# Optimization experiments

Hardware: AMD Instinct MI355X
Metric: run time of the kernel (lower is better)

Reference implementation:

```python
import jax, jax.numpy as jnp
import numpy as np

B = 512
N = 8732  # SSD300 default box count, hard-coded in the original asserts


def point_form(boxes):
    # (cx, cy, w, h) -> (xmin, ymin, xmax, ymax), as in the original repo
    return jnp.concatenate([boxes[..., :2] - boxes[..., 2:] / 2,
                            boxes[..., :2] + boxes[..., 2:] / 2], axis=-1)


def setup_inputs() -> dict:
    key = jax.random.key(0)
    k1, k2, k3, k4, k5 = jax.random.split(key, 5)
    ploc = jax.random.normal(k1, (B, 4, N), jnp.float32)
    pconf = jax.random.normal(k2, (B, 2, N), jnp.float32)
    # ground-truth boxes: keep w/h strictly positive for the log in _to_offsets
    gloc = jax.random.uniform(k3, (B, N, 4), jnp.float32, minval=0.05, maxval=1.0)
    glabel = (jax.random.uniform(k4, (B, N)) < 0.02).astype(jnp.int32)
    # default boxes in cxcywh; keep away from 0 so point_form xmax/ymax > 0
    dboxes = jax.random.uniform(k5, (N, 4), jnp.float32, minval=0.2, maxval=0.8)
    return {"ploc": ploc, "pconf": pconf, "gloc": gloc, "glabel": glabel, "dboxes": dboxes}


def reference(ploc, pconf, gloc, glabel, dboxes):
    db = point_form(dboxes)                      # [N,4]
    dxy, dwh = db[:, :2], db[:, 2:]              # faithful to original indexing
    # offset encode ground truth
    gxy = (gloc[..., :2] - dxy) / dwh            # [B,N,2]
    gwh = jnp.log(gloc[..., 2:] / dwh)           # [B,N,2]
    goff = jnp.concatenate([gxy, gwh], axis=-1)  # [B,N,4]

    pl = jnp.swapaxes(ploc, 1, 2)                # [B,N,4]
    diff = pl - goff
    ad = jnp.abs(diff)
    sl1 = jnp.where(ad < 1.0, 0.5 * diff * diff, ad - 0.5).sum(-1)  # [B,N]

    mask = glabel > 0                            # [B,N]
    pos = mask.sum(axis=1)                       # [B]
    loc_loss = jnp.where(mask, sl1, 0.0).sum(axis=1)

    # per-anchor cross entropy over the class dim
    logp = jax.nn.log_softmax(pconf, axis=1)     # [B,2,N]
    closs = -jnp.take_along_axis(logp, glabel[:, None, :], axis=1)[:, 0, :]  # [B,N]

    # hard negative mining: rank negatives by loss via double argsort
    con_neg = jnp.where(mask, 0.0, closs)
    con_idx = jnp.argsort(-con_neg, axis=1)
    con_rank = jnp.argsort(con_idx, axis=1)
    neg_num = jnp.minimum(3 * pos, N)[:, None]
    neg_mask = con_rank < neg_num
    w = mask.astype(closs.dtype) + neg_mask.astype(closs.dtype)
    con_loss = (closs * w).sum(axis=1)

    total = loc_loss + con_loss
    num_mask = (pos > 0).astype(total.dtype)
    posf = jnp.maximum(pos.astype(total.dtype), 1e-6)
    return (total * num_mask / posf).mean()
```

## Files before the change

### kernel.cpp

```cpp
#include <hip/hip_runtime.h>
#include <cstdint>

#define BLOCK 1024
#define NWAVES (BLOCK/64)
#define NHIST 8
#define B_SZ 512
#define N_SZ 8732
#define NG (N_SZ/4)

__device__ __forceinline__ float f4c(const float4& v, int j) {
  return j==0 ? v.x : (j==1 ? v.y : (j==2 ? v.z : v.w));
}
__device__ __forceinline__ int i4c(const int4& v, int j) {
  return j==0 ? v.x : (j==1 ? v.y : (j==2 ? v.z : v.w));
}
__device__ __forceinline__ float smoothl1(float d) {
  float ad = fabsf(d);
  return ad < 1.0f ? 0.5f*d*d : ad - 0.5f;
}

__global__ __launch_bounds__(BLOCK, 8)
void mbl_row_kernel(const float* __restrict__ ploc,
                    const float* __restrict__ pconf,
                    const float* __restrict__ gloc,
                    const int*   __restrict__ glabel,
                    const float* __restrict__ dboxes,
                    float* __restrict__ rowout)
{
  __shared__ __align__(16) uint32_t con[N_SZ];
  __shared__ uint32_t hist[NHIST*256];
  __shared__ float redf[NWAVES], redf2[NWAVES];
  __shared__ int   redi[NWAVES];
  __shared__ int sh_pos, sh_rem;
  __shared__ uint32_t sh_prefix;
  __shared__ float sh_loc, sh_pcl;

  const int b    = blockIdx.x;
  const int tid  = threadIdx.x;
  const int wid  = tid >> 6;
  const int lane = tid & 63;

  const float* pl  = ploc  + (size_t)b * (4*N_SZ);
  const float* pc  = pconf + (size_t)b * (2*N_SZ);
  const float4* gl4  = (const float4*)(gloc   + (size_t)b * (N_SZ*4));
  const int4*   lab4 = (const int4*)  (glabel + (size_t)b * N_SZ);
  const float4* db4  = (const float4*)dboxes;

  for (int i = tid; i < NHIST*256; i += BLOCK) hist[i] = 0u;
  __syncthreads();

  float loc_acc = 0.f, pcl_acc = 0.f;
  int pos_acc = 0;
  uint32_t* hmy = hist + (wid & (NHIST-1))*256;

  for (int g = tid; g < NG; g += BLOCK) {
    const int n = g*4;
    float4 pl0 = *(const float4*)(pl + n);
    float4 pl1 = *(const float4*)(pl + N_SZ   + n);
    float4 pl2 = *(const float4*)(pl + 2*N_SZ + n);
    float4 pl3 = *(const float4*)(pl + 3*N_SZ + n);
    float4 pc0 = *(const float4*)(pc + n);
    float4 pc1 = *(const float4*)(pc + N_SZ + n);
    int4 lb = lab4[g];
    uint32_t cw[4];
    #pragma unroll
    for (int j = 0; j < 4; ++j) {
      float4 g4 = gl4[n + j];
      float4 d4 = db4[n + j];
      float dxy0 = d4.x - 0.5f*d4.z;
      float dxy1 = d4.y - 0.5f*d4.w;
      float dwh0 = d4.x + 0.5f*d4.z;
      float dwh1 = d4.y + 0.5f*d4.w;
      float go0 = __fdividef(g4.x - dxy0, dwh0);
      float go1 = __fdividef(g4.y - dxy1, dwh1);
      float go2 = __logf(__fdividef(g4.z, dwh0));
      float go3 = __logf(__fdividef(g4.w, dwh1));
      float s = smoothl1(f4c(pl0,j) - go0)
              + smoothl1(f4c(pl1,j) - go1)
              + smoothl1(f4c(pl2,j) - go2)
              + smoothl1(f4c(pl3,j) - go3);
      float x0 = f4c(pc0,j), x1 = f4c(pc1,j);
      float d  = x1 - x0;
      float sp = __logf(1.0f + __expf(-fabsf(d)));
      int L = i4c(lb, j);
      float closs = sp + (L ? fmaxf(-d, 0.f) : fmaxf(d, 0.f));
      if (L > 0) {
        pos_acc += 1;
        loc_acc += s;
        pcl_acc += closs;
        cw[j] = 0u;
      } else {
        cw[j] = __float_as_uint(closs);
      }
    }
    ((uint4*)con)[g] = make_uint4(cw[0], cw[1], cw[2], cw[3]);
    atomicAdd(&hmy[cw[0] >> 24], 1u);
    atomicAdd(&hmy[cw[1] >> 24], 1u);
    atomicAdd(&hmy[cw[2] >> 24], 1u);
    atomicAdd(&hmy[cw[3] >> 24], 1u);
  }

  #pragma unroll
  for (int off = 32; off; off >>= 1) {
    loc_acc += __shfl_down(loc_acc, off);
    pcl_acc += __shfl_down(pcl_acc, off);
    pos_acc += __shfl_down(pos_acc, off);
  }
  if (lane == 0) { redf[wid] = loc_acc; redf2[wid] = pcl_acc; redi[wid] = pos_acc; }
  __syncthreads();
  if (tid == 0) {
    float lsum = 0.f, psum = 0.f; int ps = 0;
    for (int w = 0; w < NWAVES; ++w) { lsum += redf[w]; psum += redf2[w]; ps += redi[w]; }
    sh_loc = lsum; sh_pcl = psum; sh_pos = ps;
    sh_prefix = 0u;
    int K = 3*ps; if (K > N_SZ) K = N_SZ;
    sh_rem = K;
  }
  __syncthreads();

  const int pos = sh_pos;
  if (pos > 0) {
    for (int shift = 24; shift >= 0; shift -= 8) {
      if (shift != 24) {
        for (int i = tid; i < NHIST*256; i += BLOCK) hist[i] = 0u;
        __syncthreads();
        const uint32_t pref  = sh_prefix;
        const uint32_t pmask = 0xFFFFFFFFu << (shift+8);
        for (int n = tid; n < N_SZ; n += BLOCK) {
          uint32_t bits = con[n];
          if ((bits & pmask) == pref)
            atomicAdd(&hmy[(bits >> shift) & 255u], 1u);
        }
        __syncthreads();
      }
      if (wid == 0) {
        uint32_t c0 = 0, c1 = 0, c2 = 0, c3 = 0;
        #pragma unroll
        for (int w = 0; w < NHIST; ++w) {
          const uint32_t* h = hist + w*256 + 4*lane;
          c0 += h[0]; c1 += h[1]; c2 += h[2]; c3 += h[3];
        }
        uint32_t sl = c0 + c1 + c2 + c3;
        uint32_t suf = sl;
        #pragma unroll
        for (int off = 1; off < 64; off <<= 1) {
          uint32_t v = __shfl_down(suf, off);
          if (lane + off < 64) suf += v;
        }
        uint32_t ex = suf - sl;
        uint32_t s3 = ex + c3;
        uint32_t s2 = s3 + c2;
        uint32_t s1 = s2 + c1;
        uint32_t s0 = s1 + c0;
        const uint32_t rem  = (uint32_t)sh_rem;
        const uint32_t pref = sh_prefix;
        if (s0 >= rem && s1 < rem) { sh_prefix = pref | ((uint32_t)(4*lane  ) << shift); sh_rem = (int)(rem - s1); }
        if (s1 >= rem && s2 < rem) { sh_prefix = pref | ((uint32_t)(4*lane+1) << shift); sh_rem = (int)(rem - s2); }
        if (s2 >= rem && s3 < rem) { sh_prefix = pref | ((uint32_t)(4*lane+2) << shift); sh_rem = (int)(rem - s3); }
        if (s3 >= rem && ex < rem) { sh_prefix = pref | ((uint32_t)(4*lane+3) << shift); sh_rem = (int)(rem - ex); }
      }
      __syncthreads();
    }

    const uint32_t tbits = sh_prefix;
    const int ties = sh_rem;
    float sg = 0.f;
    for (int n = tid; n < N_SZ; n += BLOCK) {
      uint32_t bits = con[n];
      if (bits > tbits) sg += __uint_as_float(bits);
    }
    #pragma unroll
    for (int off = 32; off; off >>= 1) sg += __shfl_down(sg, off);
    if (lane == 0) redf[wid] = sg;
    __syncthreads();
    if (tid == 0) {
      float sum_gt = 0.f;
      for (int w = 0; w < NWAVES; ++w) sum_gt += redf[w];
      float con_loss = sh_pcl + sum_gt + (float)ties * __uint_as_float(tbits);
      float total = sh_loc + con_loss;
      rowout[b] = total / (float)pos;
    }
  } else {
    if (tid == 0) rowout[b] = 0.f;
  }
}

__global__ void mbl_reduce(const float* __restrict__ rowv, float* __restrict__ out) {
  __shared__ float red[8];
  const int tid = threadIdx.x;
  float v = (tid < B_SZ) ? rowv[tid] : 0.f;
  #pragma unroll
  for (int off = 32; off; off >>= 1) v += __shfl_down(v, off);
  if ((tid & 63) == 0) red[tid >> 6] = v;
  __syncthreads();
  if (tid == 0) {
    float s = 0.f;
    for (int w = 0; w < 8; ++w) s += red[w];
    out[0] = s / (float)B_SZ;
  }
}

extern "C" void kernel_launch(void* const* d_in, const int* in_sizes, int n_in,
                              void* d_out, int out_size, void* d_ws, size_t ws_size,
                              hipStream_t stream) {
  const float* ploc   = (const float*)d_in[0];
  const float* pconf  = (const float*)d_in[1];
  const float* gloc   = (const float*)d_in[2];
  const int*   glabel = (const int*)  d_in[3];
  const float* dboxes = (const float*)d_in[4];
  float* rowv = (float*)d_ws;

  hipLaunchKernelGGL(mbl_row_kernel, dim3(B_SZ), dim3(BLOCK), 0, stream,
                     ploc, pconf, gloc, glabel, dboxes, rowv);
  hipLaunchKernelGGL(mbl_reduce, dim3(1), dim3(512), 0, stream,
                     rowv, (float*)d_out);
}
```

Before: 197.5 us.

## Compact top-byte candidates to shrink later radix-select passes

After the first histogram pass selects the threshold's top byte, elements with that byte are compacted into a shared candidate buffer via ballot-based allocation, and elements above it are summed in the same sweep. Subsequent 8-bit radix passes and the final greater-than sum scan only the candidates instead of all anchors. This adds a second N-sized shared array, raising LDS use per block and possibly reducing occupancy.

```diff
diff --git a/kernel.cpp b/kernel.cpp
--- a/kernel.cpp
+++ b/kernel.cpp
@@ -17,6 +17,34 @@
 __device__ __forceinline__ float smoothl1(float d) {
   float ad = fabsf(d);
   return ad < 1.0f ? 0.5f*d*d : ad - 0.5f;
+}
+
+__device__ __forceinline__ void wave_select(const uint32_t* hbase, int ncop,
+                                            int lane, int shift,
+                                            uint32_t* shp, int* shr)
+{
+  uint32_t c0=0, c1=0, c2=0, c3=0;
+  for (int w = 0; w < ncop; ++w) {
+    const uint32_t* h = hbase + w*256 + 4*lane;
+    c0 += h[0]; c1 += h[1]; c2 += h[2]; c3 += h[3];
+  }
+  uint32_t sl = c0+c1+c2+c3, suf = sl;
+  #pragma unroll
+  for (int off = 1; off < 64; off <<= 1) {
+    uint32_t v = __shfl_down(suf, off);
+    if (lane + off < 64) suf += v;
+  }
+  uint32_t ex = suf - sl;
+  uint32_t s3 = ex + c3;
+  uint32_t s2 = s3 + c2;
+  uint32_t s1 = s2 + c1;
+  uint32_t s0 = s1 + c0;
+  const uint32_t rem  = (uint32_t)*shr;
+  const uint32_t pref = *shp;
+  if (s0 >= rem && s1 < rem) { *shp = pref | ((uint32_t)(4*lane  ) << shift); *shr = (int)(rem - s1); }
+  if (s1 >= rem && s2 < rem) { *shp = pref | ((uint32_t)(4*lane+1) << shift); *shr = (int)(rem - s2); }
+  if (s2 >= rem && s3 < rem) { *shp = pref | ((uint32_t)(4*lane+2) << shift); *shr = (int)(rem - s3); }
+  if (s3 >= rem && ex < rem) { *shp = pref | ((uint32_t)(4*lane+3) << shift); *shr = (int)(rem - ex); }
 }
 
 __global__ __launch_bounds__(BLOCK, 8)
@@ -28,10 +56,12 @@
                     float* __restrict__ rowout)
 {
   __shared__ __align__(16) uint32_t con[N_SZ];
+  __shared__ __align__(16) uint32_t cand[N_SZ];
   __shared__ uint32_t hist[NHIST*256];
   __shared__ float redf[NWAVES], redf2[NWAVES];
   __shared__ int   redi[NWAVES];
   __shared__ int sh_pos, sh_rem;
+  __shared__ unsigned int sh_cnt;
   __shared__ uint32_t sh_prefix;
   __shared__ float sh_loc, sh_pcl;
 
@@ -120,58 +150,76 @@
 
   const int pos = sh_pos;
   if (pos > 0) {
-    for (int shift = 24; shift >= 0; shift -= 8) {
-      if (shift != 24) {
-        for (int i = tid; i < NHIST*256; i += BLOCK) hist[i] = 0u;
-        __syncthreads();
-        const uint32_t pref  = sh_prefix;
-        const uint32_t pmask = 0xFFFFFFFFu << (shift+8);
-        for (int n = tid; n < N_SZ; n += BLOCK) {
-          uint32_t bits = con[n];
-          if ((bits & pmask) == pref)
-            atomicAdd(&hmy[(bits >> shift) & 255u], 1u);
+    if (wid == 0) wave_select(hist, NHIST, lane, 24, &sh_prefix, &sh_rem);
+    if (tid == BLOCK-1) sh_cnt = 0u;
+    __syncthreads();
+
+    const uint32_t d1 = sh_prefix >> 24;
+    float sgacc = 0.f;
+
+    if (tid < 256) hist[tid] = 0u;
+    for (int n = tid; n < N_SZ; n += BLOCK) {
+      uint32_t bits = con[n];
+      uint32_t top = bits >> 24;
+      if (top > d1) sgacc += __uint_as_float(bits);
+      bool take = (top == d1);
+      uint64_t tmask = __ballot(take);
+      if (tmask) {
+        uint64_t amask = __ballot(true);
+        int leader = __ffsll((unsigned long long)amask) - 1;
+        uint32_t base = 0;
+        if (lane == leader) base = atomicAdd(&sh_cnt, (unsigned int)__popcll(tmask));
+        base = __shfl(base, leader);
+        if (take) {
+          int off = __popcll(tmask & ((1ull << lane) - 1ull));
+          cand[base + off] = bits;
         }
-        __syncthreads();
-      }
-      if (wid == 0) {
-        uint32_t c0 = 0, c1 = 0, c2 = 0, c3 = 0;
-        #pragma unroll
-        for (int w = 0; w < NHIST; ++w) {
-          const uint32_t* h = hist + w*256 + 4*lane;
-          c0 += h[0]; c1 += h[1]; c2 += h[2]; c3 += h[3];
-        }
-        uint32_t sl = c0 + c1 + c2 + c3;
-        uint32_t suf = sl;
-        #pragma unroll
-        for (int off = 1; off < 64; off <<= 1) {
-          uint32_t v = __shfl_down(suf, off);
-          if (lane + off < 64) suf += v;
-        }
-        uint32_t ex = suf - sl;
-        uint32_t s3 = ex + c3;
-        uint32_t s2 = s3 + c2;
-        uint32_t s1 = s2 + c1;
-        uint32_t s0 = s1 + c0;
-        const uint32_t rem  = (uint32_t)sh_rem;
-        const uint32_t pref = sh_prefix;
-        if (s0 >= rem && s1 < rem) { sh_prefix = pref | ((uint32_t)(4*lane  ) << shift); sh_rem = (int)(rem - s1); }
-        if (s1 >= rem && s2 < rem) { sh_prefix = pref | ((uint32_t)(4*lane+1) << shift); sh_rem = (int)(rem - s2); }
-        if (s2 >= rem && s3 < rem) { sh_prefix = pref | ((uint32_t)(4*lane+2) << shift); sh_rem = (int)(rem - s3); }
-        if (s3 >= rem && ex < rem) { sh_prefix = pref | ((uint32_t)(4*lane+3) << shift); sh_rem = (int)(rem - ex); }
-      }
-      __syncthreads();
-    }
+      }
+    }
+    __syncthreads();
+    const int cnt = (int)sh_cnt;
+
+    for (int i = tid; i < cnt; i += BLOCK)
+      atomicAdd(&hist[(cand[i] >> 16) & 255u], 1u);
+    __syncthreads();
+    if (wid == 0) wave_select(hist, 1, lane, 16, &sh_prefix, &sh_rem);
+    if (tid >= 256 && tid < 512) hist[tid] = 0u;
+    __syncthreads();
+
+    {
+      const uint32_t p2 = sh_prefix & 0xFFFF0000u;
+      for (int i = tid; i < cnt; i += BLOCK) {
+        uint32_t v = cand[i];
+        if ((v & 0xFFFF0000u) == p2)
+          atomicAdd(&hist[256 + ((v >> 8) & 255u)], 1u);
+      }
+    }
+    __syncthreads();
+    if (wid == 0) wave_select(hist + 256, 1, lane, 8, &sh_prefix, &sh_rem);
+    if (tid >= 256 && tid < 512) hist[tid - 256] = 0u;
+    __syncthreads();
+
+    {
+      const uint32_t p3 = sh_prefix & 0xFFFFFF00u;
+      for (int i = tid; i < cnt; i += BLOCK) {
+        uint32_t v = cand[i];
+        if ((v & 0xFFFFFF00u) == p3)
+          atomicAdd(&hist[v & 255u], 1u);
+      }
+    }
+    __syncthreads();
+    if (wid == 0) wave_select(hist, 1, lane, 0, &sh_prefix, &sh_rem);
+    __syncthreads();
 
     const uint32_t tbits = sh_prefix;
     const int ties = sh_rem;
-    float sg = 0.f;
-    for (int n = tid; n < N_SZ; n += BLOCK) {
-      uint32_t bits = con[n];
-      if (bits > tbits) sg += __uint_as_float(bits);
+    for (int i = tid; i < cnt; i += BLOCK) {
+      uint32_t v = cand[i];
+      if (v > tbits) sgacc += __uint_as_float(v);
     }
     #pragma unroll
-    for (int off = 32; off; off >>= 1) sg += __shfl_down(sg, off);
-    if (lane == 0) redf[wid] = sg;
+    for (int off = 32; off; off >>= 1) sgacc += __shfl_down(sgacc, off);
+    if (lane == 0) redf[wid] = sgacc;
     __syncthreads();
     if (tid == 0) {
       float sum_gt = 0.f;
```

Result: no change. 197.9 us (+0.2%).
